# Kernel tuning notes

Hardware: AMD Instinct MI355X
Metric: run time of the kernel (lower is better)

The kernel has to match this reference:

```python
import jax, jax.numpy as jnp
import numpy as np


def _maxpool2(x):
    # 2x2 max pool, stride 2; x: [B, C, H, W]
    B, C, H, W = x.shape
    return x.reshape(B, C, H // 2, 2, W // 2, 2).max(axis=(3, 5))


def setup_inputs() -> dict:
    key = jax.random.key(0)
    ks = jax.random.split(key, 6)
    B, C, H, W = 8, 256, 64, 64
    x = jax.random.normal(ks[0], (B, C, H, W), dtype=jnp.float32)
    w_theta = jax.random.normal(ks[1], (C // 8, C), dtype=jnp.float32) * (C ** -0.5)
    w_phi = jax.random.normal(ks[2], (C // 8, C), dtype=jnp.float32) * (C ** -0.5)
    w_g = jax.random.normal(ks[3], (C // 2, C), dtype=jnp.float32) * (C ** -0.5)
    w_o = jax.random.normal(ks[4], (C, C // 2), dtype=jnp.float32) * ((C // 2) ** -0.5)
    gamma = jnp.ones((), dtype=jnp.float32)
    return {"x": x, "w_theta": w_theta, "w_phi": w_phi, "w_g": w_g, "w_o": w_o, "gamma": gamma}


def reference(x, w_theta, w_phi, w_g, w_o, gamma):
    B, C, H, W = x.shape
    N = H * W
    # 1x1 convs are channel-mixing matmuls
    theta = jnp.einsum('oc,bchw->bohw', w_theta, x).reshape(B, C // 8, N)        # [B, C/8, N]
    phi = _maxpool2(jnp.einsum('oc,bchw->bohw', w_phi, x)).reshape(B, C // 8, N // 4)  # [B, C/8, N/4]
    g = _maxpool2(jnp.einsum('oc,bchw->bohw', w_g, x)).reshape(B, C // 2, N // 4)      # [B, C/2, N/4]
    # attention: softmax(theta^T phi) over pooled key axis
    beta = jax.nn.softmax(jnp.einsum('bcn,bcm->bnm', theta, phi), axis=-1)       # [B, N, N/4]
    o = jnp.einsum('bcm,bnm->bcn', g, beta).reshape(B, C // 2, H, W)             # [B, C/2, H, W]
    o = jnp.einsum('oc,bchw->bohw', w_o, o)                                      # [B, C, H, W]
    return gamma * o + x
```

## Files before the change

### kernel.cpp

```cpp
#include <hip/hip_runtime.h>

#define B_ 8
#define C_ 256
#define N_ 4096
#define CK 32
#define CG 128
#define M_ 1024

typedef __attribute__((ext_vector_type(8))) short bf16x8;
typedef __attribute__((ext_vector_type(4))) float f32x4;

__device__ __forceinline__ short f2bf(float f) {
  union { float f; unsigned u; } v; v.f = f;
  unsigned r = (v.u + 0x7FFF + ((v.u >> 16) & 1)) >> 16;
  return (short)r;
}
__device__ __forceinline__ int packbf2(float a, float b) {
  return (f2bf(a) & 0xFFFF) | (f2bf(b) << 16);
}
__device__ __forceinline__ int cvtpk(float lo, float hi) {
  int r;
  asm("v_cvt_pk_bf16_f32 %0, %1, %2" : "=v"(r) : "v"(lo), "v"(hi));
  return r;
}

__global__ __launch_bounds__(256) void prep_kernel(const float* __restrict__ wt,
                                                   const float* __restrict__ wp,
                                                   const float* __restrict__ wg,
                                                   const float* __restrict__ wo,
                                                   short* __restrict__ wcat,
                                                   short* __restrict__ wo_bf) {
  int i = (blockIdx.x * 256 + threadIdx.x) * 4;
  const float* src;
  short* dst;
  int off;
  if (i < 8192)        { src = wt; dst = wcat;         off = i; }
  else if (i < 16384)  { src = wp; dst = wcat + 8192;  off = i - 8192; }
  else if (i < 49152)  { src = wg; dst = wcat + 16384; off = i - 16384; }
  else                 { src = wo; dst = wo_bf;        off = i - 49152; }
  float4 v = *(const float4*)(src + off);
  int2 p;
  p.x = packbf2(v.x, v.y);
  p.y = packbf2(v.z, v.w);
  *(int2*)(dst + off) = p;
}

__global__ __launch_bounds__(512) void proj_kernel(const float* __restrict__ x,
                                                   const short* __restrict__ wcat,
                                                   short* __restrict__ theta_t,
                                                   short* __restrict__ phi_t,
                                                   short* __restrict__ g_bf) {
  __shared__ __align__(16) short w_s[192 * 256];
  __shared__ __align__(16) short x_s[64 * 256];
  int tid = threadIdx.x;
  int bx = blockIdx.x, b = blockIdx.y;
  int t = bx >> 1, half = bx & 1;

#pragma unroll
  for (int rep = 0; rep < 12; ++rep) {
    int idx = rep * 512 + tid;
    int o = idx >> 5, gp = idx & 31;
    int4 v = *(const int4*)&wcat[o * 256 + gp * 8];
    *(int4*)&w_s[o * 256 + ((gp ^ (o & 7)) * 8)] = v;
  }
  {
    int l = tid & 63, cq = tid >> 6;
    int xoff = l >> 1, dy = l & 1;
    int n = t * 128 + dy * 64 + half * 32 + xoff;
    const float* xb = x + (size_t)b * C_ * N_ + n;
#pragma unroll
    for (int rep = 0; rep < 2; ++rep) {
      int ch = cq + rep * 8;
      int c0 = ch * 16;
      float f[16];
#pragma unroll
      for (int i = 0; i < 16; ++i) f[i] = xb[(size_t)(c0 + i) * N_];
      int4 pa, pb;
      pa.x = cvtpk(f[0], f[1]);   pa.y = cvtpk(f[2], f[3]);
      pa.z = cvtpk(f[4], f[5]);   pa.w = cvtpk(f[6], f[7]);
      pb.x = cvtpk(f[8], f[9]);   pb.y = cvtpk(f[10], f[11]);
      pb.z = cvtpk(f[12], f[13]); pb.w = cvtpk(f[14], f[15]);
      *(int4*)&x_s[l * 256 + (((2 * ch) ^ (l & 7)) * 8)] = pa;
      *(int4*)&x_s[l * 256 + (((2 * ch + 1) ^ (l & 7)) * 8)] = pb;
    }
  }
  __syncthreads();

  int lane = tid & 63, w = tid >> 6;
  int h = lane >> 4, q = lane & 15;
  int ns = w & 3, ow = w >> 2;
  f32x4 acc[6];
#pragma unroll
  for (int j = 0; j < 6; ++j) acc[j] = (f32x4){0.f, 0.f, 0.f, 0.f};

  int nl = 16 * ns + q;
#pragma unroll
  for (int ks = 0; ks < 8; ++ks) {
    bf16x8 bfr = *(const bf16x8*)&x_s[nl * 256 + (((4 * ks + h) ^ (nl & 7)) * 8)];
#pragma unroll
    for (int j = 0; j < 6; ++j) {
      int o = 16 * (6 * ow + j) + q;
      bf16x8 afr = *(const bf16x8*)&w_s[o * 256 + (((4 * ks + h) ^ (o & 7)) * 8)];
      acc[j] = __builtin_amdgcn_mfma_f32_16x16x32_bf16(afr, bfr, acc[j], 0, 0, 0);
    }
  }

  int xoff = nl >> 1, dy = nl & 1;
  int n = t * 128 + dy * 64 + half * 32 + xoff;
  int m = t * 32 + half * 16 + (nl >> 2);
#pragma unroll
  for (int j = 0; j < 6; ++j) {
    int ot = 6 * ow + j;
    if (ot < 2) {
      int2 pp;
      pp.x = cvtpk(acc[j][0], acc[j][1]);
      pp.y = cvtpk(acc[j][2], acc[j][3]);
      *(int2*)&theta_t[((size_t)b * N_ + n) * CK + ot * 16 + 4 * h] = pp;
    } else {
      float v[4];
#pragma unroll
      for (int r = 0; r < 4; ++r) {
        float vv = acc[j][r];
        vv = fmaxf(vv, __shfl_xor(vv, 1));
        vv = fmaxf(vv, __shfl_xor(vv, 2));
        v[r] = vv;
      }
      if ((nl & 3) == 0) {
        if (ot < 4) {
          int2 pp;
          pp.x = cvtpk(v[0], v[1]);
          pp.y = cvtpk(v[2], v[3]);
          *(int2*)&phi_t[((size_t)b * M_ + m) * CK + (ot - 2) * 16 + 4 * h] = pp;
        } else {
#pragma unroll
          for (int r = 0; r < 4; ++r) {
            int oc = (ot - 4) * 16 + 4 * h + r;
            g_bf[((size_t)b * CG + oc) * M_ + m] = f2bf(v[r]);
          }
        }
      }
    }
  }
}

__global__ __launch_bounds__(512, 1) void attn_out_kernel(const short* __restrict__ theta_t,
                                                          const short* __restrict__ phi_t,
                                                          const short* __restrict__ g_bf,
                                                          const short* __restrict__ wo_bf,
                                                          const float* __restrict__ x,
                                                          const float* __restrict__ gamma,
                                                          float* __restrict__ out) {
  __shared__ __align__(16) short lds[50176];
  short* phi_s = lds;
  short* g_sA = lds + 5120;
  short* p_sb = lds + 23552;

  int tid = threadIdx.x;
  int lane = tid & 63, w = tid >> 6;
  int h = lane >> 4, q = lane & 15;
  int bid = blockIdx.x;
  int b = bid & 7, n0 = (bid >> 3) * 128;
  int n = n0 + 16 * w + q;
  float gm = gamma[0];

  bf16x8 qfrag = *(const bf16x8*)&theta_t[((size_t)b * N_ + n) * CK + 8 * h];

  f32x4 Oacc[8];
#pragma unroll
  for (int ct = 0; ct < 8; ++ct) Oacc[ct] = (f32x4){0.f, 0.f, 0.f, 0.f};
  float Mx = -INFINITY, S = 0.f;
  const f32x4 zero4 = {0.f, 0.f, 0.f, 0.f};

  int pm_ = tid >> 2, pc_ = tid & 3;
  int gc0 = tid >> 3, gm0 = tid & 7;
  int gc1 = (512 + tid) >> 3, gm1 = tid & 7;
  short* p_sw = p_sb + w * 1152;

  if (tid < 256)
    *(int4*)&phi_s[pm_ * 40 + 8 * pc_] =
        *(const int4*)&phi_t[((size_t)b * M_ + pm_) * CK + 8 * pc_];
  *(int4*)&g_sA[gc0 * 72 + 8 * gm0] =
      *(const int4*)&g_bf[((size_t)b * CG + gc0) * M_ + 8 * gm0];
  *(int4*)&g_sA[gc1 * 72 + 8 * gm1] =
      *(const int4*)&g_bf[((size_t)b * CG + gc1) * M_ + 8 * gm1];
  __syncthreads();

  for (int it = 0; it < 16; ++it) {
    int cur = it & 1;
    short* phi_c = phi_s + cur * 2560;
    short* g_c = g_sA + cur * 9216;
    int4 rphi, rg0, rg1;
    if (it < 15) {
      int m0n = (it + 1) * 64;
      if (tid < 256)
        rphi = *(const int4*)&phi_t[((size_t)b * M_ + m0n + pm_) * CK + 8 * pc_];
      rg0 = *(const int4*)&g_bf[((size_t)b * CG + gc0) * M_ + m0n + 8 * gm0];
      rg1 = *(const int4*)&g_bf[((size_t)b * CG + gc1) * M_ + m0n + 8 * gm1];
    }

    f32x4 pt[4];
#pragma unroll
    for (int mt = 0; mt < 4; ++mt) {
      bf16x8 af = *(const bf16x8*)&phi_c[(16 * mt + q) * 40 + 8 * h];
      pt[mt] = __builtin_amdgcn_mfma_f32_16x16x32_bf16(af, qfrag, zero4, 0, 0, 0);
    }

    float pm = pt[0][0];
#pragma unroll
    for (int mt = 0; mt < 4; ++mt)
#pragma unroll
      for (int r = 0; r < 4; ++r) pm = fmaxf(pm, pt[mt][r]);
    pm = fmaxf(pm, __shfl_xor(pm, 16));
    pm = fmaxf(pm, __shfl_xor(pm, 32));
    if (!__all(pm - Mx <= 8.f)) {
      float Mn = fmaxf(Mx, pm);
      float fsc = __expf(Mx - Mn);
      S *= fsc;
#pragma unroll
      for (int ct = 0; ct < 8; ++ct) Oacc[ct] *= fsc;
      Mx = Mn;
    }
    float ps = 0.f;
#pragma unroll
    for (int mt = 0; mt < 4; ++mt) {
      float e0 = __expf(pt[mt][0] - Mx);
      float e1 = __expf(pt[mt][1] - Mx);
      float e2 = __expf(pt[mt][2] - Mx);
      float e3 = __expf(pt[mt][3] - Mx);
      ps += (e0 + e1) + (e2 + e3);
      int2 pk;
      pk.x = cvtpk(e0, e1);
      pk.y = cvtpk(e2, e3);
      *(int2*)&p_sw[q * 72 + 16 * mt + 4 * h] = pk;
    }
    ps += __shfl_xor(ps, 16);
    ps += __shfl_xor(ps, 32);
    S += ps;

    __builtin_amdgcn_s_setprio(1);
#pragma unroll
    for (int kp = 0; kp < 2; ++kp) {
      bf16x8 pf = *(const bf16x8*)&p_sw[q * 72 + 32 * kp + 8 * h];
#pragma unroll
      for (int ct = 0; ct < 8; ++ct) {
        bf16x8 vf = *(const bf16x8*)&g_c[(16 * ct + q) * 72 + 32 * kp + 8 * h];
        Oacc[ct] = __builtin_amdgcn_mfma_f32_16x16x32_bf16(vf, pf, Oacc[ct], 0, 0, 0);
      }
    }
    __builtin_amdgcn_s_setprio(0);

    if (it < 15) {
      int nxt = cur ^ 1;
      if (tid < 256) *(int4*)&phi_s[nxt * 2560 + pm_ * 40 + 8 * pc_] = rphi;
      *(int4*)&g_sA[nxt * 9216 + gc0 * 72 + 8 * gm0] = rg0;
      *(int4*)&g_sA[nxt * 9216 + gc1 * 72 + 8 * gm1] = rg1;
    }
    __syncthreads();
  }

  short* ot_s = lds;
  short* wo_s = lds + 17408;
  float rS = 1.f / S;
  int nloc = 16 * w + q;
#pragma unroll
  for (int ct = 0; ct < 8; ++ct) {
    int2 pp;
    pp.x = cvtpk(Oacc[ct][0] * rS, Oacc[ct][1] * rS);
    pp.y = cvtpk(Oacc[ct][2] * rS, Oacc[ct][3] * rS);
    *(int2*)&ot_s[nloc * 136 + 16 * ct + 4 * h] = pp;
  }
#pragma unroll
  for (int rep = 0; rep < 8; ++rep) {
    int idx = rep * 512 + tid;
    int o = idx >> 4, gp = idx & 15;
    int4 v = *(const int4*)&wo_bf[o * 128 + gp * 8];
    *(int4*)&wo_s[o * 128 + ((gp ^ (o & 7)) * 8)] = v;
  }
  __syncthreads();

  int nq = w & 3, oh = w >> 2;
  f32x4 acc[8][2];
#pragma unroll
  for (int j = 0; j < 8; ++j)
#pragma unroll
    for (int nn = 0; nn < 2; ++nn) acc[j][nn] = (f32x4){0.f, 0.f, 0.f, 0.f};

#pragma unroll
  for (int ks = 0; ks < 4; ++ks) {
    bf16x8 bfr0 = *(const bf16x8*)&ot_s[(32 * nq + q) * 136 + 32 * ks + 8 * h];
    bf16x8 bfr1 = *(const bf16x8*)&ot_s[(32 * nq + 16 + q) * 136 + 32 * ks + 8 * h];
#pragma unroll
    for (int j = 0; j < 8; ++j) {
      int o = 128 * oh + 16 * j + q;
      bf16x8 afr = *(const bf16x8*)&wo_s[o * 128 + (((4 * ks + h) ^ (o & 7)) * 8)];
      acc[j][0] = __builtin_amdgcn_mfma_f32_16x16x32_bf16(afr, bfr0, acc[j][0], 0, 0, 0);
      acc[j][1] = __builtin_amdgcn_mfma_f32_16x16x32_bf16(afr, bfr1, acc[j][1], 0, 0, 0);
    }
  }

#pragma unroll
  for (int j = 0; j < 8; ++j)
#pragma unroll
    for (int nn = 0; nn < 2; ++nn)
#pragma unroll
      for (int r = 0; r < 4; ++r) {
        int o = 128 * oh + 16 * j + 4 * h + r;
        int nn2 = n0 + 32 * nq + 16 * nn + q;
        size_t idx = ((size_t)b * C_ + o) * N_ + nn2;
        out[idx] = gm * acc[j][nn][r] + x[idx];
      }
}

extern "C" void kernel_launch(void* const* d_in, const int* in_sizes, int n_in,
                              void* d_out, int out_size, void* d_ws, size_t ws_size,
                              hipStream_t stream) {
  const float* x = (const float*)d_in[0];
  const float* wt = (const float*)d_in[1];
  const float* wp = (const float*)d_in[2];
  const float* wg = (const float*)d_in[3];
  const float* wo = (const float*)d_in[4];
  const float* gamma = (const float*)d_in[5];
  float* out = (float*)d_out;

  short* theta_t = (short*)d_ws;
  short* phi_t = theta_t + (size_t)B_ * N_ * CK;
  short* g_bf = phi_t + (size_t)B_ * M_ * CK;
  short* wcat = g_bf + (size_t)B_ * CG * M_;
  short* wo_bf = wcat + 192 * 256;

  prep_kernel<<<dim3(80), 256, 0, stream>>>(wt, wp, wg, wo, wcat, wo_bf);
  proj_kernel<<<dim3(64, 8), 512, 0, stream>>>(x, wcat, theta_t, phi_t, g_bf);
  attn_out_kernel<<<dim3(256), 512, 0, stream>>>(theta_t, phi_t, g_bf, wo_bf, x, gamma, out);
}
```

Before: 59.07 us.

## Fuse weight bf16 conversion into consumers and widen attention key tile to 128

Removes the separate prep kernel by converting fp32 weights to bf16 inside proj_kernel and attn_out_kernel as they are staged into LDS, which saves one launch and a global round trip. The attention loop now processes 128 keys per iteration instead of 64, halving the iteration count. The g tile becomes single-buffered with an extra barrier before refill, while phi stays double-buffered. This trades less loop and softmax-rescale overhead for more registers, larger prefetch staging and more synchronisation per step. Each block also now converts the weights redundantly.

```diff
diff --git a/kernel.cpp b/kernel.cpp
--- a/kernel.cpp
+++ b/kernel.cpp
@@ -15,38 +15,16 @@
   unsigned r = (v.u + 0x7FFF + ((v.u >> 16) & 1)) >> 16;
   return (short)r;
 }
-__device__ __forceinline__ int packbf2(float a, float b) {
-  return (f2bf(a) & 0xFFFF) | (f2bf(b) << 16);
-}
 __device__ __forceinline__ int cvtpk(float lo, float hi) {
   int r;
   asm("v_cvt_pk_bf16_f32 %0, %1, %2" : "=v"(r) : "v"(lo), "v"(hi));
   return r;
 }
 
-__global__ __launch_bounds__(256) void prep_kernel(const float* __restrict__ wt,
+__global__ __launch_bounds__(512) void proj_kernel(const float* __restrict__ x,
+                                                   const float* __restrict__ wt,
                                                    const float* __restrict__ wp,
                                                    const float* __restrict__ wg,
-                                                   const float* __restrict__ wo,
-                                                   short* __restrict__ wcat,
-                                                   short* __restrict__ wo_bf) {
-  int i = (blockIdx.x * 256 + threadIdx.x) * 4;
-  const float* src;
-  short* dst;
-  int off;
-  if (i < 8192)        { src = wt; dst = wcat;         off = i; }
-  else if (i < 16384)  { src = wp; dst = wcat + 8192;  off = i - 8192; }
-  else if (i < 49152)  { src = wg; dst = wcat + 16384; off = i - 16384; }
-  else                 { src = wo; dst = wo_bf;        off = i - 49152; }
-  float4 v = *(const float4*)(src + off);
-  int2 p;
-  p.x = packbf2(v.x, v.y);
-  p.y = packbf2(v.z, v.w);
-  *(int2*)(dst + off) = p;
-}
-
-__global__ __launch_bounds__(512) void proj_kernel(const float* __restrict__ x,
-                                                   const short* __restrict__ wcat,
                                                    short* __restrict__ theta_t,
                                                    short* __restrict__ phi_t,
                                                    short* __restrict__ g_bf) {
@@ -60,8 +38,15 @@
   for (int rep = 0; rep < 12; ++rep) {
     int idx = rep * 512 + tid;
     int o = idx >> 5, gp = idx & 31;
-    int4 v = *(const int4*)&wcat[o * 256 + gp * 8];
-    *(int4*)&w_s[o * 256 + ((gp ^ (o & 7)) * 8)] = v;
+    const float* src = (o < 32) ? (wt + o * 256)
+                     : (o < 64) ? (wp + (o - 32) * 256)
+                                : (wg + (o - 64) * 256);
+    float4 f0 = *(const float4*)(src + gp * 8);
+    float4 f1 = *(const float4*)(src + gp * 8 + 4);
+    int4 pk;
+    pk.x = cvtpk(f0.x, f0.y); pk.y = cvtpk(f0.z, f0.w);
+    pk.z = cvtpk(f1.x, f1.y); pk.w = cvtpk(f1.z, f1.w);
+    *(int4*)&w_s[o * 256 + ((gp ^ (o & 7)) * 8)] = pk;
   }
   {
     int l = tid & 63, cq = tid >> 6;
@@ -146,14 +131,14 @@
 __global__ __launch_bounds__(512, 1) void attn_out_kernel(const short* __restrict__ theta_t,
                                                           const short* __restrict__ phi_t,
                                                           const short* __restrict__ g_bf,
-                                                          const short* __restrict__ wo_bf,
+                                                          const float* __restrict__ wo,
                                                           const float* __restrict__ x,
                                                           const float* __restrict__ gamma,
                                                           float* __restrict__ out) {
   __shared__ __align__(16) short lds[50176];
   short* phi_s = lds;
-  short* g_sA = lds + 5120;
-  short* p_sb = lds + 23552;
+  short* g_s = lds + 10240;
+  short* p_sb = lds + 27648;
 
   int tid = threadIdx.x;
   int lane = tid & 63, w = tid >> 6;
@@ -172,42 +157,43 @@
   const f32x4 zero4 = {0.f, 0.f, 0.f, 0.f};
 
   int pm_ = tid >> 2, pc_ = tid & 3;
-  int gc0 = tid >> 3, gm0 = tid & 7;
-  int gc1 = (512 + tid) >> 3, gm1 = tid & 7;
-  short* p_sw = p_sb + w * 1152;
-
-  if (tid < 256)
-    *(int4*)&phi_s[pm_ * 40 + 8 * pc_] =
-        *(const int4*)&phi_t[((size_t)b * M_ + pm_) * CK + 8 * pc_];
-  *(int4*)&g_sA[gc0 * 72 + 8 * gm0] =
-      *(const int4*)&g_bf[((size_t)b * CG + gc0) * M_ + 8 * gm0];
-  *(int4*)&g_sA[gc1 * 72 + 8 * gm1] =
-      *(const int4*)&g_bf[((size_t)b * CG + gc1) * M_ + 8 * gm1];
+  int gm_ = tid & 15;
+  short* p_sw = p_sb + w * 2176;
+
+  *(int4*)&phi_s[pm_ * 40 + 8 * pc_] =
+      *(const int4*)&phi_t[((size_t)b * M_ + pm_) * CK + 8 * pc_];
+#pragma unroll
+  for (int k = 0; k < 4; ++k) {
+    int gc = (k * 512 + tid) >> 4;
+    *(int4*)&g_s[gc * 136 + 8 * gm_] =
+        *(const int4*)&g_bf[((size_t)b * CG + gc) * M_ + 8 * gm_];
+  }
   __syncthreads();
 
-  for (int it = 0; it < 16; ++it) {
+  for (int it = 0; it < 8; ++it) {
     int cur = it & 1;
-    short* phi_c = phi_s + cur * 2560;
-    short* g_c = g_sA + cur * 9216;
-    int4 rphi, rg0, rg1;
-    if (it < 15) {
-      int m0n = (it + 1) * 64;
-      if (tid < 256)
-        rphi = *(const int4*)&phi_t[((size_t)b * M_ + m0n + pm_) * CK + 8 * pc_];
-      rg0 = *(const int4*)&g_bf[((size_t)b * CG + gc0) * M_ + m0n + 8 * gm0];
-      rg1 = *(const int4*)&g_bf[((size_t)b * CG + gc1) * M_ + m0n + 8 * gm1];
-    }
-
-    f32x4 pt[4];
-#pragma unroll
-    for (int mt = 0; mt < 4; ++mt) {
+    const short* phi_c = phi_s + cur * 5120;
+    int4 rphi, rg[4];
+    if (it < 7) {
+      int m0n = (it + 1) * 128;
+      rphi = *(const int4*)&phi_t[((size_t)b * M_ + m0n + pm_) * CK + 8 * pc_];
+#pragma unroll
+      for (int k = 0; k < 4; ++k) {
+        int gc = (k * 512 + tid) >> 4;
+        rg[k] = *(const int4*)&g_bf[((size_t)b * CG + gc) * M_ + m0n + 8 * gm_];
+      }
+    }
+
+    f32x4 pt[8];
+#pragma unroll
+    for (int mt = 0; mt < 8; ++mt) {
       bf16x8 af = *(const bf16x8*)&phi_c[(16 * mt + q) * 40 + 8 * h];
       pt[mt] = __builtin_amdgcn_mfma_f32_16x16x32_bf16(af, qfrag, zero4, 0, 0, 0);
     }
 
     float pm = pt[0][0];
 #pragma unroll
-    for (int mt = 0; mt < 4; ++mt)
+    for (int mt = 0; mt < 8; ++mt)
 #pragma unroll
       for (int r = 0; r < 4; ++r) pm = fmaxf(pm, pt[mt][r]);
     pm = fmaxf(pm, __shfl_xor(pm, 16));
@@ -222,7 +208,7 @@
     }
     float ps = 0.f;
 #pragma unroll
-    for (int mt = 0; mt < 4; ++mt) {
+    for (int mt = 0; mt < 8; ++mt) {
       float e0 = __expf(pt[mt][0] - Mx);
       float e1 = __expf(pt[mt][1] - Mx);
       float e2 = __expf(pt[mt][2] - Mx);
@@ -231,7 +217,7 @@
       int2 pk;
       pk.x = cvtpk(e0, e1);
       pk.y = cvtpk(e2, e3);
-      *(int2*)&p_sw[q * 72 + 16 * mt + 4 * h] = pk;
+      *(int2*)&p_sw[q * 136 + 16 * mt + 4 * h] = pk;
     }
     ps += __shfl_xor(ps, 16);
     ps += __shfl_xor(ps, 32);
@@ -239,23 +225,26 @@
 
     __builtin_amdgcn_s_setprio(1);
 #pragma unroll
-    for (int kp = 0; kp < 2; ++kp) {
-      bf16x8 pf = *(const bf16x8*)&p_sw[q * 72 + 32 * kp + 8 * h];
+    for (int kp = 0; kp < 4; ++kp) {
+      bf16x8 pf = *(const bf16x8*)&p_sw[q * 136 + 32 * kp + 8 * h];
 #pragma unroll
       for (int ct = 0; ct < 8; ++ct) {
-        bf16x8 vf = *(const bf16x8*)&g_c[(16 * ct + q) * 72 + 32 * kp + 8 * h];
+        bf16x8 vf = *(const bf16x8*)&g_s[(16 * ct + q) * 136 + 32 * kp + 8 * h];
         Oacc[ct] = __builtin_amdgcn_mfma_f32_16x16x32_bf16(vf, pf, Oacc[ct], 0, 0, 0);
       }
     }
     __builtin_amdgcn_s_setprio(0);
 
-    if (it < 15) {
-      int nxt = cur ^ 1;
-      if (tid < 256) *(int4*)&phi_s[nxt * 2560 + pm_ * 40 + 8 * pc_] = rphi;
-      *(int4*)&g_sA[nxt * 9216 + gc0 * 72 + 8 * gm0] = rg0;
-      *(int4*)&g_sA[nxt * 9216 + gc1 * 72 + 8 * gm1] = rg1;
-    }
     __syncthreads();
+    if (it < 7) {
+      *(int4*)&phi_s[(cur ^ 1) * 5120 + pm_ * 40 + 8 * pc_] = rphi;
+#pragma unroll
+      for (int k = 0; k < 4; ++k) {
+        int gc = (k * 512 + tid) >> 4;
+        *(int4*)&g_s[gc * 136 + 8 * gm_] = rg[k];
+      }
+      __syncthreads();
+    }
   }
 
   short* ot_s = lds;
@@ -273,8 +262,12 @@
   for (int rep = 0; rep < 8; ++rep) {
     int idx = rep * 512 + tid;
     int o = idx >> 4, gp = idx & 15;
-    int4 v = *(const int4*)&wo_bf[o * 128 + gp * 8];
-    *(int4*)&wo_s[o * 128 + ((gp ^ (o & 7)) * 8)] = v;
+    float4 f0 = *(const float4*)(wo + o * 128 + gp * 8);
+    float4 f1 = *(const float4*)(wo + o * 128 + gp * 8 + 4);
+    int4 pk;
+    pk.x = cvtpk(f0.x, f0.y); pk.y = cvtpk(f0.z, f0.w);
+    pk.z = cvtpk(f1.x, f1.y); pk.w = cvtpk(f1.z, f1.w);
+    *(int4*)&wo_s[o * 128 + ((gp ^ (o & 7)) * 8)] = pk;
   }
   __syncthreads();
 
@@ -325,10 +318,7 @@
   short* theta_t = (short*)d_ws;
   short* phi_t = theta_t + (size_t)B_ * N_ * CK;
   short* g_bf = phi_t + (size_t)B_ * M_ * CK;
-  short* wcat = g_bf + (size_t)B_ * CG * M_;
-  short* wo_bf = wcat + 192 * 256;
-
-  prep_kernel<<<dim3(80), 256, 0, stream>>>(wt, wp, wg, wo, wcat, wo_bf);
-  proj_kernel<<<dim3(64, 8), 512, 0, stream>>>(x, wcat, theta_t, phi_t, g_bf);
-  attn_out_kernel<<<dim3(256), 512, 0, stream>>>(theta_t, phi_t, g_bf, wo_bf, x, gamma, out);
-}
+
+  proj_kernel<<<dim3(64, 8), 512, 0, stream>>>(x, wt, wp, wg, theta_t, phi_t, g_bf);
+  attn_out_kernel<<<dim3(256), 512, 0, stream>>>(theta_t, phi_t, g_bf, wo, x, gamma, out);
+}
```

After: 78.03 us. +32.1%, slower.
